# Kernel tuning notes

Measured on AMD Instinct MI355X. Metric: run time of the kernel, lower is better.

Reference implementation:

```python
import jax, jax.numpy as jnp
import numpy as np

C = 64                      # num_channels
NUM_BLOCKS = 8
DILATIONS = [1, 2, 4, 8, 16, 32, 64, 128]
KS = 2                      # kernel_size
MAX_NUM_SAMPLES = 4096
NC = 3                      # num_components
IN_CH = 1


def causal_conv(x, w, b, dilation):
    # x: [B, Cin, T], w: [Cout, Cin, K] (torch OIH layout), left-pad for causality
    pad = (w.shape[-1] - 1) * dilation
    y = jax.lax.conv_general_dilated(
        x, w, window_strides=(1,), padding=[(pad, 0)],
        rhs_dilation=(dilation,), dimension_numbers=('NCH', 'OIH', 'NCH'))
    return y + b[None, :, None]


def conv1x1(x, w, b):
    # w: [Cout, Cin, 1]
    return jnp.einsum('oc,bct->bot', w[:, :, 0], x) + b[None, :, None]


def setup_inputs() -> dict:
    key = jax.random.key(0)
    ks = jax.random.split(key, 16)
    s = 0.1
    inp = {
        'x': jax.random.normal(ks[0], (64, IN_CH, 4096), dtype=jnp.float32),
        'w_in': s * jax.random.normal(ks[1], (C, IN_CH + 1, KS), dtype=jnp.float32),
        'b_in': s * jax.random.normal(ks[2], (C,), dtype=jnp.float32),
        'blk_w1': s * jax.random.normal(ks[3], (NUM_BLOCKS, 2 * C, C, KS), dtype=jnp.float32),
        'blk_b1': s * jax.random.normal(ks[4], (NUM_BLOCKS, 2 * C), dtype=jnp.float32),
        'blk_w2': s * jax.random.normal(ks[5], (NUM_BLOCKS, C, C, 1), dtype=jnp.float32),
        'blk_b2': s * jax.random.normal(ks[6], (NUM_BLOCKS, C), dtype=jnp.float32),
        'w_mid': s * jax.random.normal(ks[7], (2 * C, C, 1), dtype=jnp.float32),
        'b_mid': s * jax.random.normal(ks[8], (2 * C,), dtype=jnp.float32),
        'w_pi': s * jax.random.normal(ks[9], (NC + 1, 2 * C, 1), dtype=jnp.float32),
        'b_pi': s * jax.random.normal(ks[10], (NC + 1,), dtype=jnp.float32),
        'w_mu': s * jax.random.normal(ks[11], (NC, 2 * C, 1), dtype=jnp.float32),
        'b_mu': s * jax.random.normal(ks[12], (NC,), dtype=jnp.float32),
        'w_sigma': s * jax.random.normal(ks[13], (NC, 2 * C, 1), dtype=jnp.float32),
        'b_sigma': s * jax.random.normal(ks[14], (NC,), dtype=jnp.float32),
    }
    return inp


def reference(x, w_in, b_in, blk_w1, blk_b1, blk_w2, blk_b2,
              w_mid, b_mid, w_pi, b_pi, w_mu, b_mu, w_sigma, b_sigma):
    B, _, T = x.shape
    # time channel: linspace(0, T/max_num_samples, T) broadcast over batch
    lins = jnp.broadcast_to(
        jnp.linspace(0.0, T / MAX_NUM_SAMPLES, T, dtype=x.dtype)[None, None, :],
        (B, 1, T))
    h = causal_conv(jnp.concatenate([x, lins], axis=1), w_in, b_in, 1)
    acc = h  # running sum of taps (taps[0] is conv1 output)
    for i in range(NUM_BLOCKS):
        a = causal_conv(h, blk_w1[i], blk_b1[i], DILATIONS[i])  # [B, 2C, T]
        gated = jnp.tanh(a[:, :C]) * jax.nn.sigmoid(a[:, C:])
        h = conv1x1(gated, blk_w2[i], blk_b2[i]) + h            # residual
        acc = acc + h
    agg = jax.nn.relu(acc / (NUM_BLOCKS + 1))  # mean of 9 taps then relu
    z = conv1x1(agg, w_mid, b_mid)             # [B, 2C, T]
    pi = jax.nn.softmax(conv1x1(z, w_pi, b_pi), axis=1)
    mu = 2.0 * jnp.tanh(conv1x1(z, w_mu, b_mu) / 2.0)
    sigma = jax.nn.softplus(conv1x1(z, w_sigma, b_sigma))
    return pi, mu, sigma
```

## Files before the change

kernel.cpp:

```cpp
#include <hip/hip_runtime.h>
#include <math.h>

#define NB 64
#define NCH 64
#define NT 4096
#define TOUT 512
#define ROWS 768

typedef float f32x4 __attribute__((ext_vector_type(4)));
typedef short s16x8 __attribute__((ext_vector_type(8)));

__device__ __forceinline__ float fast_rcp(float x) { return __builtin_amdgcn_rcpf(x); }
__device__ __forceinline__ float fast_sigmoid(float x) { return fast_rcp(1.0f + __expf(-x)); }
__device__ __forceinline__ float fast_tanh(float x) {
    return 1.0f - 2.0f * fast_rcp(__expf(2.0f * x) + 1.0f);
}
__device__ __forceinline__ unsigned short f2bf(float f) {
    unsigned int u = __builtin_bit_cast(unsigned int, f);
    u += 0x7fffu + ((u >> 16) & 1u);
    return (unsigned short)(u >> 16);
}
__device__ __forceinline__ float bf2f_lo(unsigned int u) { return __builtin_bit_cast(float, u << 16); }
__device__ __forceinline__ float bf2f_hi(unsigned int u) { return __builtin_bit_cast(float, u & 0xffff0000u); }

#define HSW(j, cb) ((j)*128 + ((cb) ^ (((j)&7) << 4)))

#define OFF_GB  98304
#define OFF_RED 98304
#define OFF_WCT 118784
#define LDS_SZ  121344

__global__ __launch_bounds__(256) void k_pack(
    const float* __restrict__ bw1, const float* __restrict__ bw2,
    short* __restrict__ w1p, short* __restrict__ w2p)
{
    const int id = blockIdx.x * 256 + threadIdx.x;
    if (id < 16384) {
        const int l = id & 63, ks = (id >> 6) & 3, mi = (id >> 8) & 1,
                  g = (id >> 9) & 3, L = id >> 11;
        const int co = 16*g + (l & 15) + 64*mi;
        short v[8];
        #pragma unroll
        for (int j = 0; j < 8; ++j) {
            const int k = 32*ks + 8*(l >> 4) + j;
            const int ci = k & 63, tap = k >> 6;
            v[j] = (short)f2bf(bw1[((size_t)(L*128 + co)*64 + ci)*2 + tap]);
        }
        *(s16x8*)(w1p + (size_t)id*8) = *(const s16x8*)v;
    } else if (id < 16384 + 4096) {
        const int id2 = id - 16384;
        const int l = id2 & 63, ks = (id2 >> 6) & 1, g = (id2 >> 7) & 3, L = id2 >> 9;
        const int co = 16*g + (l & 15);
        short v[8];
        #pragma unroll
        for (int j = 0; j < 8; ++j) {
            const int ci = 32*ks + 8*(l >> 4) + j;
            v[j] = (short)f2bf(bw2[(size_t)(L*64 + co)*64 + ci]);
        }
        *(s16x8*)(w2p + (size_t)id2*8) = *(const s16x8*)v;
    }
}

__global__ void k_compose(
    const float* __restrict__ w_mid, const float* __restrict__ b_mid,
    const float* __restrict__ w_pi,  const float* __restrict__ b_pi,
    const float* __restrict__ w_mu,  const float* __restrict__ b_mu,
    const float* __restrict__ w_sg,  const float* __restrict__ b_sg,
    float* __restrict__ wct, float* __restrict__ bc)
{
    const int tid = threadIdx.x;
    if (tid < 640) {
        const int o = tid >> 6, c = tid & 63;
        const float* wh = (o < 4) ? (w_pi + o*128)
                        : (o < 7) ? (w_mu + (o-4)*128) : (w_sg + (o-7)*128);
        float s = 0.f;
        for (int j = 0; j < 128; ++j) s += wh[j] * w_mid[j*64 + c];
        wct[c*10 + o] = s * (1.0f/9.0f);
    }
    if (tid < 10) {
        const int o = tid;
        const float* wh = (o < 4) ? (w_pi + o*128)
                        : (o < 7) ? (w_mu + (o-4)*128) : (w_sg + (o-7)*128);
        const float bh = (o < 4) ? b_pi[o] : (o < 7) ? b_mu[o-4] : b_sg[o-7];
        float s = bh;
        for (int j = 0; j < 128; ++j) s += wh[j] * b_mid[j];
        bc[o] = s;
    }
}

#define CHUNK_BODY(TC, USEREG, CC)                                              \
  {                                                                             \
    f32x4 accf0[4], accf1[4];                                                   \
    _Pragma("unroll")                                                           \
    for (int nf = 0; nf < 4; ++nf) {                                            \
      accf0[nf] = (f32x4){0.f,0.f,0.f,0.f};                                     \
      accf1[nf] = (f32x4){0.f,0.f,0.f,0.f};                                     \
    }                                                                           \
    _Pragma("unroll")                                                           \
    for (int nf = 0; nf < 4; ++nf) {                                            \
      const int rb = (TC) + 64*th + 16*nf + l15;                                \
      _Pragma("unroll")                                                         \
      for (int ks = 0; ks < 4; ++ks) {                                          \
        int jr = rb - d + (ks >> 1)*d;                  \
        jr = jr < 0 ? 0 : jr;                \
        const int cb = 64*(ks & 1) + 16*lq;                                     \
        const s16x8 bf = *(const s16x8*)(lds + HSW(jr, cb));                    \
        accf0[nf] = __builtin_amdgcn_mfma_f32_16x16x32_bf16(a1[0][ks], bf, accf0[nf], 0,0,0); \
        accf1[nf] = __builtin_amdgcn_mfma_f32_16x16x32_bf16(a1[1][ks], bf, accf1[nf], 0,0,0); \
      }                                                                         \
    }                                                                           \
    _Pragma("unroll")                                                           \
    for (int nf = 0; nf < 4; ++nf) {                                            \
      const int tl = 64*th + 16*nf + l15;                                       \
      unsigned short gg[4];                                                     \
      _Pragma("unroll")                                                         \
      for (int rr = 0; rr < 4; ++rr)                                            \
        gg[rr] = f2bf(fast_tanh(accf0[nf][rr] + bt[rr]) *                       \
                      fast_sigmoid(accf1[nf][rr] + bs[rr]));                    \
      uint2 pk;                                                                 \
      pk.x = (unsigned int)gg[0] | ((unsigned int)gg[1] << 16);                 \
      pk.y = (unsigned int)gg[2] | ((unsigned int)gg[3] << 16);                 \
      *(uint2*)(lds + OFF_GB + HSW(tl, 2*cobase)) = pk;                         \
    }                                                                           \
    __syncthreads();                                                            \
    f32x4 c2[4];                                                                \
    _Pragma("unroll")                                                           \
    for (int nf = 0; nf < 4; ++nf) c2[nf] = (f32x4){0.f,0.f,0.f,0.f};           \
    _Pragma("unroll")                                                           \
    for (int nf = 0; nf < 4; ++nf) {                                            \
      const int tl = 64*th + 16*nf + l15;                                       \
      _Pragma("unroll")                                                         \
      for (int ks = 0; ks < 2; ++ks) {                                          \
        const int cb = 64*ks + 16*lq;                                           \
        const s16x8 bf = *(const s16x8*)(lds + OFF_GB + HSW(tl, cb));           \
        c2[nf] = __builtin_amdgcn_mfma_f32_16x16x32_bf16(a2[ks], bf, c2[nf], 0,0,0); \
      }                                                                         \
    }                                                                           \
    _Pragma("unroll")                                                           \
    for (int nf = 0; nf < 4; ++nf) {                                            \
      const int r  = (TC) + 64*th + 16*nf + l15;                                \
      const int ha = HSW(r, 2*cobase);                                          \
      f32x4 resid;                                                              \
      if (USEREG) {                                                             \
        resid = h_reg[CC][nf];                                                  \
      } else {                                                                  \
        const uint2 hp = *(const uint2*)(lds + ha);                             \
        resid[0] = bf2f_lo(hp.x); resid[1] = bf2f_hi(hp.x);                     \
        resid[2] = bf2f_lo(hp.y); resid[3] = bf2f_hi(hp.y);                     \
      }                                                                         \
      f32x4 hn;                                                                 \
      _Pragma("unroll")                                                         \
      for (int rr = 0; rr < 4; ++rr) hn[rr] = c2[nf][rr] + b2v[rr] + resid[rr]; \
      if (USEREG) {                                                             \
        h_reg[CC][nf] = hn;                                                     \
        _Pragma("unroll")                                                       \
        for (int rr = 0; rr < 4; ++rr) acc_reg[CC][nf][rr] += hn[rr];           \
      }                                                                         \
      uint2 po;                                                                 \
      po.x = (unsigned int)f2bf(hn[0]) | ((unsigned int)f2bf(hn[1]) << 16);     \
      po.y = (unsigned int)f2bf(hn[2]) | ((unsigned int)f2bf(hn[3]) << 16);     \
      if (t0 + r < 256) { po.x = 0u; po.y = 0u; }   \
      *(uint2*)(lds + ha) = po;                                                 \
    }                                                                           \
    __syncthreads();                                                            \
  }

__global__ __launch_bounds__(512, 2) void k_mega(
    const short* __restrict__ w1p, const float* __restrict__ bb1,
    const short* __restrict__ w2p, const float* __restrict__ bb2,
    const float* __restrict__ w_in, const float* __restrict__ b_in,
    const float* __restrict__ x,
    const float* __restrict__ wct, const float* __restrict__ bc,
    float* __restrict__ out)
{
    __shared__ __align__(16) unsigned char lds[LDS_SZ];
    const int b   = blockIdx.x;
    const int t0  = blockIdx.y * TOUT;
    const int tid = threadIdx.x;
    const int w   = tid >> 6;
    const int l   = tid & 63;
    const int l15 = l & 15, lq = l >> 4;
    const int wg  = w & 3;
    const int th  = w >> 2;
    const int cobase = 16*wg + 4*lq;
    const float inv = 1.0f / 4095.0f;

    float* xs = (float*)(lds + OFF_GB);
    for (int idx = tid; idx < ROWS + 1; idx += 512) {
        const int t = t0 - 257 + idx;
        xs[idx] = (t >= 0) ? x[(size_t)b*NT + t] : 0.f;
    }
    __syncthreads();

    #pragma unroll
    for (int pp = 0; pp < 4; ++pp) {
        const int cp = w*4 + pp, c0 = 2*cp;
        const float wa0=w_in[c0*4+0], wa1=w_in[c0*4+1], wa2=w_in[c0*4+2], wa3=w_in[c0*4+3], ba=b_in[c0];
        const float wb0=w_in[c0*4+4], wb1=w_in[c0*4+5], wb2=w_in[c0*4+6], wb3=w_in[c0*4+7], bb=b_in[c0+1];
        for (int j = l; j < ROWS; j += 64) {
            const int t = t0 - 256 + j;
            float v0 = 0.f, v1 = 0.f;
            if (t >= 0) {
                const float x1v = xs[j+1], x0v = xs[j];
                const float l1v = (float)t * inv;
                const float l0v = (t > 0) ? (float)(t-1)*inv : 0.f;
                v0 = ba + wa0*x0v + wa1*x1v + wa2*l0v + wa3*l1v;
                v1 = bb + wb0*x0v + wb1*x1v + wb2*l0v + wb3*l1v;
            }
            *(unsigned int*)(lds + HSW(j, 4*cp)) =
                (unsigned int)f2bf(v0) | ((unsigned int)f2bf(v1) << 16);
        }
    }

    f32x4 h_reg[4][4], acc_reg[4][4];
    {
        float wi0[4], wi1[4], wi2[4], wi3[4], bi[4];
        #pragma unroll
        for (int rr = 0; rr < 4; ++rr) {
            const int co = cobase + rr;
            wi0[rr]=w_in[co*4+0]; wi1[rr]=w_in[co*4+1];
            wi2[rr]=w_in[co*4+2]; wi3[rr]=w_in[co*4+3]; bi[rr]=b_in[co];
        }
        #pragma unroll
        for (int cc = 0; cc < 4; ++cc) {
            #pragma unroll
            for (int nf = 0; nf < 4; ++nf) {
                const int j = 256 + 128*cc + 64*th + 16*nf + l15;
                const int t = t0 - 256 + j;
                const float x1v = xs[j+1], x0v = xs[j];
                const float l1v = (float)t * inv;
                const float l0v = (t > 0) ? (float)(t-1)*inv : 0.f;
                f32x4 hv;
                #pragma unroll
                for (int rr = 0; rr < 4; ++rr)
                    hv[rr] = bi[rr] + wi0[rr]*x0v + wi1[rr]*x1v + wi2[rr]*l0v + wi3[rr]*l1v;
                h_reg[cc][nf] = hv;
                acc_reg[cc][nf] = hv;
            }
        }
    }
    __syncthreads();

    for (int li = 0; li < 8; ++li) {
        const int d = 1 << li;
        const short* w1l = w1p + li*16384;
        const short* w2l = w2p + li*4096;
        s16x8 a1[2][4], a2[2];
        #pragma unroll
        for (int mi = 0; mi < 2; ++mi)
            #pragma unroll
            for (int ks = 0; ks < 4; ++ks)
                a1[mi][ks] = *(const s16x8*)(w1l + (size_t)(((wg*2 + mi)*4 + ks)*64 + l)*8);
        #pragma unroll
        for (int ks = 0; ks < 2; ++ks)
            a2[ks] = *(const s16x8*)(w2l + (size_t)((wg*2 + ks)*64 + l)*8);
        float bt[4], bs[4], b2v[4];
        #pragma unroll
        for (int rr = 0; rr < 4; ++rr) {
            bt[rr]  = bb1[li*128 + cobase + rr];
            bs[rr]  = bb1[li*128 + 64 + cobase + rr];
            b2v[rr] = bb2[li*64 + cobase + rr];
        }

        #pragma unroll
        for (int cci = 0; cci < 4; ++cci) {
            const int cc = 3 - cci;
            CHUNK_BODY(256 + 128*cc, 1, cc)
        }
        if (li <= 6) CHUNK_BODY(128, 0, 0)
        if (li <= 5) CHUNK_BODY(0,   0, 0)
    }

    float* wcl = (float*)(lds + OFF_WCT);
    for (int i = tid; i < 640; i += 512) wcl[i] = wct[i];
    __syncthreads();
    float* red = (float*)(lds + OFF_RED);
    #pragma unroll
    for (int cc = 0; cc < 4; ++cc) {
        #pragma unroll
        for (int nf = 0; nf < 4; ++nf) {
            float p[10];
            #pragma unroll
            for (int o = 0; o < 10; ++o) p[o] = 0.f;
            #pragma unroll
            for (int rr = 0; rr < 4; ++rr) {
                float a = acc_reg[cc][nf][rr];
                a = a > 0.f ? a : 0.f;
                const float* wr = wcl + (cobase + rr)*10;
                #pragma unroll
                for (int o = 0; o < 10; ++o) p[o] += wr[o] * a;
            }
            #pragma unroll
            for (int o = 0; o < 10; ++o) {
                p[o] += __shfl_xor(p[o], 16, 64);
                p[o] += __shfl_xor(p[o], 32, 64);
            }
            if (lq == 0) {
                const int tl = 64*th + 16*nf + l15;
                #pragma unroll
                for (int o = 0; o < 10; ++o) red[(wg*128 + tl)*10 + o] = p[o];
            }
        }
        __syncthreads();
        if (tid < 128) {
            float hd[10];
            #pragma unroll
            for (int o = 0; o < 10; ++o)
                hd[o] = bc[o] + red[(0*128+tid)*10+o] + red[(1*128+tid)*10+o]
                              + red[(2*128+tid)*10+o] + red[(3*128+tid)*10+o];
            const int t = t0 + 128*cc + tid;
            const float m  = fmaxf(fmaxf(hd[0], hd[1]), fmaxf(hd[2], hd[3]));
            const float e0 = __expf(hd[0]-m), e1 = __expf(hd[1]-m);
            const float e2 = __expf(hd[2]-m), e3 = __expf(hd[3]-m);
            const float rs = fast_rcp(e0+e1+e2+e3);
            const size_t piBase = (size_t)(b*4)*NT + t;
            out[piBase       ] = e0*rs;
            out[piBase +  NT ] = e1*rs;
            out[piBase + 2*NT] = e2*rs;
            out[piBase + 3*NT] = e3*rs;
            float* muO = out + (size_t)NB*4*NT;
            float* sgO = out + (size_t)NB*7*NT;
            #pragma unroll
            for (int o = 0; o < 3; ++o) {
                muO[(size_t)(b*3+o)*NT + t] = 2.0f * fast_tanh(0.5f * hd[4+o]);
                const float sv = hd[7+o];
                sgO[(size_t)(b*3+o)*NT + t] = (sv > 15.0f) ? sv : logf(1.0f + __expf(sv));
            }
        }
        __syncthreads();
    }
}

extern "C" void kernel_launch(void* const* d_in, const int* in_sizes, int n_in,
                              void* d_out, int out_size, void* d_ws, size_t ws_size,
                              hipStream_t stream)
{
    const float* x     = (const float*)d_in[0];
    const float* w_in  = (const float*)d_in[1];
    const float* b_in  = (const float*)d_in[2];
    const float* bw1   = (const float*)d_in[3];
    const float* bb1   = (const float*)d_in[4];
    const float* bw2   = (const float*)d_in[5];
    const float* bb2   = (const float*)d_in[6];
    const float* w_mid = (const float*)d_in[7];
    const float* b_mid = (const float*)d_in[8];
    const float* w_pi  = (const float*)d_in[9];
    const float* b_pi  = (const float*)d_in[10];
    const float* w_mu  = (const float*)d_in[11];
    const float* b_mu  = (const float*)d_in[12];
    const float* w_sg  = (const float*)d_in[13];
    const float* b_sg  = (const float*)d_in[14];
    float* out = (float*)d_out;

    short* w1p = (short*)d_ws;
    short* w2p = w1p + 8*16384;
    float* wct = (float*)(w2p + 8*4096);
    float* bcp = wct + 640;

    k_pack<<<80, 256, 0, stream>>>(bw1, bw2, w1p, w2p);
    k_compose<<<1, 1024, 0, stream>>>(w_mid, b_mid, w_pi, b_pi, w_mu, b_mu,
                                      w_sg, b_sg, wct, bcp);
    k_mega<<<dim3(NB, NT/TOUT), 512, 0, stream>>>(
        w1p, bb1, w2p, bb2, w_in, b_in, x, wct, bcp, out);
}
```

Measured before the change: 377.0 us.

## Use 1024-thread blocks with LDS-staged conv weights and double-buffered gate tile

Doubles the workgroup to 16 waves, so each wave covers 32 time rows instead of 64 and holds half the accumulator registers. Per-layer dilated-conv weights are staged into LDS once per block rather than held per wave in registers. The gated-activation buffer alternates between two LDS regions, which removes the trailing barrier after each chunk. This is meant to raise parallelism and relieve register pressure, but it adds LDS traffic for weight reads, uses a larger LDS footprint (one block per CU), and reads the head weights from global memory instead of LDS.

```diff
diff --git a/kernel.cpp b/kernel.cpp
--- a/kernel.cpp
+++ b/kernel.cpp
@@ -25,10 +25,10 @@
 
 #define HSW(j, cb) ((j)*128 + ((cb) ^ (((j)&7) << 4)))
 
-#define OFF_GB  98304
-#define OFF_RED 98304
-#define OFF_WCT 118784
-#define LDS_SZ  121344
+#define OFF_GB0 98304
+#define OFF_GB1 114688
+#define OFF_W   131072
+#define LDS_SZ  163840
 
 __global__ __launch_bounds__(256) void k_pack(
     const float* __restrict__ bw1, const float* __restrict__ bw2,
@@ -90,55 +90,54 @@
 
 #define CHUNK_BODY(TC, USEREG, CC)                                              \
   {                                                                             \
-    f32x4 accf0[4], accf1[4];                                                   \
+    const int gof = gsel ? OFF_GB1 : OFF_GB0;                                   \
+    f32x4 acg0[2], acg1[2];                                                     \
+    acg0[0] = (f32x4){0.f,0.f,0.f,0.f}; acg0[1] = (f32x4){0.f,0.f,0.f,0.f};     \
+    acg1[0] = (f32x4){0.f,0.f,0.f,0.f}; acg1[1] = (f32x4){0.f,0.f,0.f,0.f};     \
     _Pragma("unroll")                                                           \
-    for (int nf = 0; nf < 4; ++nf) {                                            \
-      accf0[nf] = (f32x4){0.f,0.f,0.f,0.f};                                     \
-      accf1[nf] = (f32x4){0.f,0.f,0.f,0.f};                                     \
-    }                                                                           \
-    _Pragma("unroll")                                                           \
-    for (int nf = 0; nf < 4; ++nf) {                                            \
-      const int rb = (TC) + 64*th + 16*nf + l15;                                \
+    for (int ks = 0; ks < 4; ++ks) {                                            \
+      const s16x8 a10 = *(const s16x8*)(lds + OFF_W + (size_t)(((cg*2+0)*4+ks)*64 + l)*16); \
+      const s16x8 a11 = *(const s16x8*)(lds + OFF_W + (size_t)(((cg*2+1)*4+ks)*64 + l)*16); \
       _Pragma("unroll")                                                         \
-      for (int ks = 0; ks < 4; ++ks) {                                          \
+      for (int nf = 0; nf < 2; ++nf) {                                          \
+        const int rb = (TC) + 32*th + 16*nf + l15;                              \
         int jr = rb - d + (ks >> 1)*d;                  \
         jr = jr < 0 ? 0 : jr;                \
         const int cb = 64*(ks & 1) + 16*lq;                                     \
         const s16x8 bf = *(const s16x8*)(lds + HSW(jr, cb));                    \
-        accf0[nf] = __builtin_amdgcn_mfma_f32_16x16x32_bf16(a1[0][ks], bf, accf0[nf], 0,0,0); \
-        accf1[nf] = __builtin_amdgcn_mfma_f32_16x16x32_bf16(a1[1][ks], bf, accf1[nf], 0,0,0); \
+        acg0[nf] = __builtin_amdgcn_mfma_f32_16x16x32_bf16(a10, bf, acg0[nf], 0,0,0); \
+        acg1[nf] = __builtin_amdgcn_mfma_f32_16x16x32_bf16(a11, bf, acg1[nf], 0,0,0); \
       }                                                                         \
     }                                                                           \
     _Pragma("unroll")                                                           \
-    for (int nf = 0; nf < 4; ++nf) {                                            \
-      const int tl = 64*th + 16*nf + l15;                                       \
+    for (int nf = 0; nf < 2; ++nf) {                                            \
+      const int tl = 32*th + 16*nf + l15;                                       \
       unsigned short gg[4];                                                     \
       _Pragma("unroll")                                                         \
       for (int rr = 0; rr < 4; ++rr)                                            \
-        gg[rr] = f2bf(fast_tanh(accf0[nf][rr] + bt[rr]) *                       \
-                      fast_sigmoid(accf1[nf][rr] + bs[rr]));                    \
+        gg[rr] = f2bf(fast_tanh(acg0[nf][rr] + bt[rr]) *                        \
+                      fast_sigmoid(acg1[nf][rr] + bs[rr]));                     \
       uint2 pk;                                                                 \
       pk.x = (unsigned int)gg[0] | ((unsigned int)gg[1] << 16);                 \
       pk.y = (unsigned int)gg[2] | ((unsigned int)gg[3] << 16);                 \
-      *(uint2*)(lds + OFF_GB + HSW(tl, 2*cobase)) = pk;                         \
+      *(uint2*)(lds + gof + HSW(tl, 2*cobase)) = pk;                            \
     }                                                                           \
     __syncthreads();                                                            \
-    f32x4 c2[4];                                                                \
+    f32x4 c2[2];                                                                \
+    c2[0] = (f32x4){0.f,0.f,0.f,0.f}; c2[1] = (f32x4){0.f,0.f,0.f,0.f};         \
     _Pragma("unroll")                                                           \
-    for (int nf = 0; nf < 4; ++nf) c2[nf] = (f32x4){0.f,0.f,0.f,0.f};           \
-    _Pragma("unroll")                                                           \
-    for (int nf = 0; nf < 4; ++nf) {                                            \
-      const int tl = 64*th + 16*nf + l15;                                       \
+    for (int ks = 0; ks < 2; ++ks) {                                            \
       _Pragma("unroll")                                                         \
-      for (int ks = 0; ks < 2; ++ks) {                                          \
+      for (int nf = 0; nf < 2; ++nf) {                                          \
+        const int tl = 32*th + 16*nf + l15;                                     \
         const int cb = 64*ks + 16*lq;                                           \
-        const s16x8 bf = *(const s16x8*)(lds + OFF_GB + HSW(tl, cb));           \
+        const s16x8 bf = *(const s16x8*)(lds + gof + HSW(tl, cb));              \
         c2[nf] = __builtin_amdgcn_mfma_f32_16x16x32_bf16(a2[ks], bf, c2[nf], 0,0,0); \
       }                                                                         \
     }                                                                           \
     _Pragma("unroll")                                                           \
-    for (int nf = 0; nf < 4; ++nf) {                                            \
-      const int r  = (TC) + 64*th + 16*nf + l15;                                \
+    for (int nf = 0; nf < 2; ++nf) {                                            \
+      const int r  = (TC) + 32*th + 16*nf + l15;                                \
       const int ha = HSW(r, 2*cobase);                                          \
       f32x4 resid;                                                              \
       if (USEREG) {                                                             \
@@ -162,10 +161,10 @@
       if (t0 + r < 256) { po.x = 0u; po.y = 0u; }   \
       *(uint2*)(lds + ha) = po;                                                 \
     }                                                                           \
-    __syncthreads();                                                            \
+    gsel ^= 1;                                                                  \
   }
 
-__global__ __launch_bounds__(512, 2) void k_mega(
+__global__ __launch_bounds__(1024) void k_mega(
     const short* __restrict__ w1p, const float* __restrict__ bb1,
     const short* __restrict__ w2p, const float* __restrict__ bb2,
     const float* __restrict__ w_in, const float* __restrict__ b_in,
@@ -180,21 +179,22 @@
     const int w   = tid >> 6;
     const int l   = tid & 63;
     const int l15 = l & 15, lq = l >> 4;
-    const int wg  = w & 3;
+    const int cg  = w & 3;
     const int th  = w >> 2;
-    const int cobase = 16*wg + 4*lq;
+    const int cobase = 16*cg + 4*lq;
     const float inv = 1.0f / 4095.0f;
-
-    float* xs = (float*)(lds + OFF_GB);
-    for (int idx = tid; idx < ROWS + 1; idx += 512) {
-        const int t = t0 - 257 + idx;
-        xs[idx] = (t >= 0) ? x[(size_t)b*NT + t] : 0.f;
+    int gsel = 0;
+
+    float* xs = (float*)(lds + OFF_GB0);
+    if (tid < ROWS + 1) {
+        const int t = t0 - 257 + tid;
+        xs[tid] = (t >= 0) ? x[(size_t)b*NT + t] : 0.f;
     }
     __syncthreads();
 
     #pragma unroll
-    for (int pp = 0; pp < 4; ++pp) {
-        const int cp = w*4 + pp, c0 = 2*cp;
+    for (int pp = 0; pp < 2; ++pp) {
+        const int cp = w*2 + pp, c0 = 2*cp;
         const float wa0=w_in[c0*4+0], wa1=w_in[c0*4+1], wa2=w_in[c0*4+2], wa3=w_in[c0*4+3], ba=b_in[c0];
         const float wb0=w_in[c0*4+4], wb1=w_in[c0*4+5], wb2=w_in[c0*4+6], wb3=w_in[c0*4+7], bb=b_in[c0+1];
         for (int j = l; j < ROWS; j += 64) {
@@ -212,7 +212,7 @@
         }
     }
 
-    f32x4 h_reg[4][4], acc_reg[4][4];
+    f32x4 h_reg[4][2], acc_reg[4][2];
     {
         float wi0[4], wi1[4], wi2[4], wi3[4], bi[4];
         #pragma unroll
@@ -224,8 +224,8 @@
         #pragma unroll
         for (int cc = 0; cc < 4; ++cc) {
             #pragma unroll
-            for (int nf = 0; nf < 4; ++nf) {
-                const int j = 256 + 128*cc + 64*th + 16*nf + l15;
+            for (int nf = 0; nf < 2; ++nf) {
+                const int j = 256 + 128*cc + 32*th + 16*nf + l15;
                 const int t = t0 - 256 + j;
                 const float x1v = xs[j+1], x0v = xs[j];
                 const float l1v = (float)t * inv;
@@ -243,17 +243,15 @@
 
     for (int li = 0; li < 8; ++li) {
         const int d = 1 << li;
-        const short* w1l = w1p + li*16384;
-        const short* w2l = w2p + li*4096;
-        s16x8 a1[2][4], a2[2];
-        #pragma unroll
-        for (int mi = 0; mi < 2; ++mi)
-            #pragma unroll
-            for (int ks = 0; ks < 4; ++ks)
-                a1[mi][ks] = *(const s16x8*)(w1l + (size_t)(((wg*2 + mi)*4 + ks)*64 + l)*8);
+        {
+            const s16x8* src = (const s16x8*)(w1p + (size_t)li*16384);
+            s16x8* dst = (s16x8*)(lds + OFF_W);
+            for (int i = tid; i < 2048; i += 1024) dst[i] = src[i];
+        }
+        s16x8 a2[2];
         #pragma unroll
         for (int ks = 0; ks < 2; ++ks)
-            a2[ks] = *(const s16x8*)(w2l + (size_t)((wg*2 + ks)*64 + l)*8);
+            a2[ks] = *(const s16x8*)(w2p + (size_t)li*4096 + (size_t)((cg*2 + ks)*64 + l)*8);
         float bt[4], bs[4], b2v[4];
         #pragma unroll
         for (int rr = 0; rr < 4; ++rr) {
@@ -261,24 +259,23 @@
             bs[rr]  = bb1[li*128 + 64 + cobase + rr];
             b2v[rr] = bb2[li*64 + cobase + rr];
         }
+        __syncthreads();
 
         #pragma unroll
         for (int cci = 0; cci < 4; ++cci) {
             const int cc = 3 - cci;
             CHUNK_BODY(256 + 128*cc, 1, cc)
         }
-        if (li <= 6) CHUNK_BODY(128, 0, 0)
-        if (li <= 5) CHUNK_BODY(0,   0, 0)
-    }
-
-    float* wcl = (float*)(lds + OFF_WCT);
-    for (int i = tid; i < 640; i += 512) wcl[i] = wct[i];
+        if (li < 7) CHUNK_BODY(128, 0, 0)
+        if (li < 6) CHUNK_BODY(0,   0, 0)
+    }
+
     __syncthreads();
-    float* red = (float*)(lds + OFF_RED);
+    float* red = (float*)(lds + OFF_GB0);
     #pragma unroll
     for (int cc = 0; cc < 4; ++cc) {
         #pragma unroll
-        for (int nf = 0; nf < 4; ++nf) {
+        for (int nf = 0; nf < 2; ++nf) {
             float p[10];
             #pragma unroll
             for (int o = 0; o < 10; ++o) p[o] = 0.f;
@@ -286,7 +283,7 @@
             for (int rr = 0; rr < 4; ++rr) {
                 float a = acc_reg[cc][nf][rr];
                 a = a > 0.f ? a : 0.f;
-                const float* wr = wcl + (cobase + rr)*10;
+                const float* wr = wct + (cobase + rr)*10;
                 #pragma unroll
                 for (int o = 0; o < 10; ++o) p[o] += wr[o] * a;
             }
@@ -296,9 +293,9 @@
                 p[o] += __shfl_xor(p[o], 32, 64);
             }
             if (lq == 0) {
-                const int tl = 64*th + 16*nf + l15;
+                const int tl = 32*th + 16*nf + l15;
                 #pragma unroll
-                for (int o = 0; o < 10; ++o) red[(wg*128 + tl)*10 + o] = p[o];
+                for (int o = 0; o < 10; ++o) red[(cg*128 + tl)*10 + o] = p[o];
             }
         }
         __syncthreads();
@@ -360,6 +357,6 @@
     k_pack<<<80, 256, 0, stream>>>(bw1, bw2, w1p, w2p);
     k_compose<<<1, 1024, 0, stream>>>(w_mid, b_mid, w_pi, b_pi, w_mu, b_mu,
                                       w_sg, b_sg, wct, bcp);
-    k_mega<<<dim3(NB, NT/TOUT), 512, 0, stream>>>(
+    k_mega<<<dim3(NB, NT/TOUT), 1024, 0, stream>>>(
         w1p, bb1, w2p, bb2, w_in, b_in, x, wct, bcp, out);
 }
```

Result: slower. 483.7 us (+28.3%).

## Halve time tile per block to fit two blocks per CU and restructure barriers

Applied to the files above, without the earlier changes.

Shrinks the per-block output tile from 512 to 256 samples, which shrinks the LDS footprint and the register arrays for h/acc so that two 512-thread blocks can be co-resident, as the launch bounds request. The gate values are now held in registers and written to LDS only after a barrier, and the trailing per-chunk barrier is moved to the start of each layer. The head weights are read straight from global memory instead of being staged in LDS. The cost is a larger share of recomputed causal halo (256 rows per 256 outputs instead of per 512), so more redundant work per block.

```diff
diff --git a/kernel.cpp b/kernel.cpp
--- a/kernel.cpp
+++ b/kernel.cpp
@@ -4,8 +4,8 @@
 #define NB 64
 #define NCH 64
 #define NT 4096
-#define TOUT 512
-#define ROWS 768
+#define TOUT 256
+#define ROWS 512
 
 typedef float f32x4 __attribute__((ext_vector_type(4)));
 typedef short s16x8 __attribute__((ext_vector_type(8)));
@@ -25,10 +25,8 @@
 
 #define HSW(j, cb) ((j)*128 + ((cb) ^ (((j)&7) << 4)))
 
-#define OFF_GB  98304
-#define OFF_RED 98304
-#define OFF_WCT 118784
-#define LDS_SZ  121344
+#define OFF_GB  65536
+#define LDS_SZ  81920
 
 __global__ __launch_bounds__(256) void k_pack(
     const float* __restrict__ bw1, const float* __restrict__ bw2,
@@ -109,20 +107,24 @@
         accf1[nf] = __builtin_amdgcn_mfma_f32_16x16x32_bf16(a1[1][ks], bf, accf1[nf], 0,0,0); \
       }                                                                         \
     }                                                                           \
-    _Pragma("unroll")                                                           \
-    for (int nf = 0; nf < 4; ++nf) {                                            \
-      const int tl = 64*th + 16*nf + l15;                                       \
+    uint2 gpk[4];                                                               \
+    _Pragma("unroll")                                                           \
+    for (int nf = 0; nf < 4; ++nf) {                                            \
       unsigned short gg[4];                                                     \
       _Pragma("unroll")                                                         \
       for (int rr = 0; rr < 4; ++rr)                                            \
         gg[rr] = f2bf(fast_tanh(accf0[nf][rr] + bt[rr]) *                       \
                       fast_sigmoid(accf1[nf][rr] + bs[rr]));                    \
-      uint2 pk;                                                                 \
-      pk.x = (unsigned int)gg[0] | ((unsigned int)gg[1] << 16);                 \
-      pk.y = (unsigned int)gg[2] | ((unsigned int)gg[3] << 16);                 \
-      *(uint2*)(lds + OFF_GB + HSW(tl, 2*cobase)) = pk;                         \
-    }                                                                           \
-    __syncthreads();                                                            \
+      gpk[nf].x = (unsigned int)gg[0] | ((unsigned int)gg[1] << 16);            \
+      gpk[nf].y = (unsigned int)gg[2] | ((unsigned int)gg[3] << 16);            \
+    }                                                                           \
+    __syncthreads();                \
+    _Pragma("unroll")                                                           \
+    for (int nf = 0; nf < 4; ++nf) {                                            \
+      const int tl = 64*th + 16*nf + l15;                                       \
+      *(uint2*)(lds + OFF_GB + HSW(tl, 2*cobase)) = gpk[nf];                    \
+    }                                                                           \
+    __syncthreads();                              \
     f32x4 c2[4];                                                                \
     _Pragma("unroll")                                                           \
     for (int nf = 0; nf < 4; ++nf) c2[nf] = (f32x4){0.f,0.f,0.f,0.f};           \
@@ -162,7 +164,6 @@
       if (t0 + r < 256) { po.x = 0u; po.y = 0u; }   \
       *(uint2*)(lds + ha) = po;                                                 \
     }                                                                           \
-    __syncthreads();                                                            \
   }
 
 __global__ __launch_bounds__(512, 2) void k_mega(
@@ -180,9 +181,9 @@
     const int w   = tid >> 6;
     const int l   = tid & 63;
     const int l15 = l & 15, lq = l >> 4;
-    const int wg  = w & 3;
+    const int cg  = w & 3;
     const int th  = w >> 2;
-    const int cobase = 16*wg + 4*lq;
+    const int cobase = 16*cg + 4*lq;
     const float inv = 1.0f / 4095.0f;
 
     float* xs = (float*)(lds + OFF_GB);
@@ -212,7 +213,7 @@
         }
     }
 
-    f32x4 h_reg[4][4], acc_reg[4][4];
+    f32x4 h_reg[2][4], acc_reg[2][4];
     {
         float wi0[4], wi1[4], wi2[4], wi3[4], bi[4];
         #pragma unroll
@@ -222,7 +223,7 @@
             wi2[rr]=w_in[co*4+2]; wi3[rr]=w_in[co*4+3]; bi[rr]=b_in[co];
         }
         #pragma unroll
-        for (int cc = 0; cc < 4; ++cc) {
+        for (int cc = 0; cc < 2; ++cc) {
             #pragma unroll
             for (int nf = 0; nf < 4; ++nf) {
                 const int j = 256 + 128*cc + 64*th + 16*nf + l15;
@@ -250,10 +251,10 @@
         for (int mi = 0; mi < 2; ++mi)
             #pragma unroll
             for (int ks = 0; ks < 4; ++ks)
-                a1[mi][ks] = *(const s16x8*)(w1l + (size_t)(((wg*2 + mi)*4 + ks)*64 + l)*8);
+                a1[mi][ks] = *(const s16x8*)(w1l + (size_t)(((cg*2 + mi)*4 + ks)*64 + l)*8);
         #pragma unroll
         for (int ks = 0; ks < 2; ++ks)
-            a2[ks] = *(const s16x8*)(w2l + (size_t)((wg*2 + ks)*64 + l)*8);
+            a2[ks] = *(const s16x8*)(w2l + (size_t)((cg*2 + ks)*64 + l)*8);
         float bt[4], bs[4], b2v[4];
         #pragma unroll
         for (int rr = 0; rr < 4; ++rr) {
@@ -261,22 +262,21 @@
             bs[rr]  = bb1[li*128 + 64 + cobase + rr];
             b2v[rr] = bb2[li*64 + cobase + rr];
         }
-
-        #pragma unroll
-        for (int cci = 0; cci < 4; ++cci) {
-            const int cc = 3 - cci;
+        __syncthreads();
+
+        #pragma unroll
+        for (int cci = 0; cci < 2; ++cci) {
+            const int cc = 1 - cci;
             CHUNK_BODY(256 + 128*cc, 1, cc)
         }
-        if (li <= 6) CHUNK_BODY(128, 0, 0)
-        if (li <= 5) CHUNK_BODY(0,   0, 0)
-    }
-
-    float* wcl = (float*)(lds + OFF_WCT);
-    for (int i = tid; i < 640; i += 512) wcl[i] = wct[i];
+        if (li < 7) CHUNK_BODY(128, 0, 0)
+        if (li < 6) CHUNK_BODY(0,   0, 0)
+    }
+
     __syncthreads();
-    float* red = (float*)(lds + OFF_RED);
+    float* red = (float*)lds;
     #pragma unroll
-    for (int cc = 0; cc < 4; ++cc) {
+    for (int cc = 0; cc < 2; ++cc) {
         #pragma unroll
         for (int nf = 0; nf < 4; ++nf) {
             float p[10];
@@ -286,7 +286,7 @@
             for (int rr = 0; rr < 4; ++rr) {
                 float a = acc_reg[cc][nf][rr];
                 a = a > 0.f ? a : 0.f;
-                const float* wr = wcl + (cobase + rr)*10;
+                const float* wr = wct + (cobase + rr)*10;
                 #pragma unroll
                 for (int o = 0; o < 10; ++o) p[o] += wr[o] * a;
             }
@@ -298,7 +298,7 @@
             if (lq == 0) {
                 const int tl = 64*th + 16*nf + l15;
                 #pragma unroll
-                for (int o = 0; o < 10; ++o) red[(wg*128 + tl)*10 + o] = p[o];
+                for (int o = 0; o < 10; ++o) red[(cg*128 + tl)*10 + o] = p[o];
             }
         }
         __syncthreads();
```

Result: slower. 417.3 us (+10.7%).
